# Optimization experiments

Measured on AMD Instinct MI355X. Metric: run time of the kernel, lower is better.

Reference implementation:

```python
import jax, jax.numpy as jnp
import numpy as np

K_ACT = 5          # k_active regimes
TAU = 0.5          # resample temperature
N = 8192           # n_particles (scaled to production size)
DZ, DM, KT, DE = 32, 64, 15, 16  # d_latent, d_mamba, k_regimes+10, d_regime_embed


def _lin(x, W, b):
    # torch nn.Linear convention: y = x @ W.T + b
    return x @ W.T + b


def setup_inputs() -> dict:
    key = jax.random.key(0)
    ks = iter(jax.random.split(key, 48))

    def rn(shape, s=1.0):
        return jax.random.normal(next(ks), shape, jnp.float32) * s

    inp = dict(
        remaining_high=jax.random.uniform(next(ks), (N,), jnp.float32) * 5.0 + 1.0,
        remaining_low=jax.random.uniform(next(ks), (N,), jnp.float32) * 5.0 + 1.0,
        z=rn((N, DZ)),
        regime_logits=rn((N, KT)),
        log_weights=rn((N,), 0.5),
        h_t=rn((DM,)),
        obs_remaining=jnp.float32(3.0),
        eps_high=rn((N,)),
        eps_low=rn((N,)),
        u_gumbel=jax.random.uniform(next(ks), (N, N), jnp.float32),
        embed=rn((KT, DE), 0.1),
        W_rt1=rn((32, DM + DE), 0.1), b_rt1=jnp.zeros(32, jnp.float32),
        W_rt2=rn((KT, 32), 0.1), b_rt2=jnp.zeros(KT, jnp.float32),
        W_d1=rn((64, DM + DE + DZ), 0.1), b_d1=jnp.zeros(64, jnp.float32),
        W_d2=rn((32, 64), 0.1), b_d2=jnp.zeros(32, jnp.float32),
        W_d3=rn((4, 32), 0.1), b_d3=jnp.zeros(4, jnp.float32),
        W_g=rn((DZ, DM + DE + DZ), 0.1), b_g=jnp.zeros(DZ, jnp.float32),
        W_c=rn((DZ, DM + DE + DZ), 0.1), b_c=jnp.zeros(DZ, jnp.float32),
        log_R=jnp.array([np.log(0.5), np.log(0.4), np.log(0.6)], jnp.float32),
        log_obs_scale=rn((KT,), 0.1),
        W_a1=rn((16, DM), 0.1), b_a1=jnp.zeros(16, jnp.float32),
        W_a2=rn((1, 16), 0.1), b_a2=jnp.zeros(1, jnp.float32),
    )
    return inp


def reference(remaining_high, remaining_low, z, regime_logits, log_weights, h_t,
              obs_remaining, eps_high, eps_low, u_gumbel, embed,
              W_rt1, b_rt1, W_rt2, b_rt2, W_d1, b_d1, W_d2, b_d2, W_d3, b_d3,
              W_g, b_g, W_c, b_c, log_R, log_obs_scale, W_a1, b_a1, W_a2, b_a2):
    silu = jax.nn.silu
    n = remaining_high.shape[0]
    h = jnp.broadcast_to(h_t, (n, h_t.shape[0]))  # (N, d_mamba)

    # ---- transition (predict step) ----
    rp = jax.nn.softmax(regime_logits, axis=-1)[:, :K_ACT]          # (N, K)
    remb = rp @ embed[:K_ACT]                                        # (N, d_embed)
    ri = jnp.concatenate([h, remb], axis=-1)                         # (N, 80)
    upd = _lin(silu(_lin(ri, W_rt1, b_rt1)), W_rt2, b_rt2)[:, :K_ACT]
    new_logits = regime_logits.at[:, :K_ACT].set(
        0.7 * regime_logits[:, :K_ACT] + 0.3 * upd)
    di = jnp.concatenate([h, remb, z], axis=-1)                      # (N, 112)
    dp = _lin(silu(_lin(silu(_lin(di, W_d1, b_d1)), W_d2, b_d2)), W_d3, b_d3)
    sig_h = jax.nn.softplus(dp[:, 2]) + 0.01
    sig_l = jax.nn.softplus(dp[:, 3]) + 0.01
    nh = jnp.clip(remaining_high + dp[:, 0] + sig_h * eps_high, 0.0)
    nl = jnp.clip(remaining_low + dp[:, 1] + sig_l * eps_low, 0.0)
    gate = jax.nn.sigmoid(_lin(di, W_g, b_g))
    nz = gate * z + (1.0 - gate) * jnp.tanh(_lin(di, W_c, b_c))

    # ---- observation: skew-normal log-likelihood (source_idx=0, 'high') ----
    R_src = jnp.clip(jnp.exp(log_R[0]), 0.15, 2.5)
    alpha = _lin(silu(_lin(h_t[None, :], W_a1, b_a1)), W_a2, b_a2)[0, 0]
    scales = jax.nn.softplus(log_obs_scale[:K_ACT])
    nrp = jax.nn.softmax(new_logits, axis=-1)[:, :K_ACT]
    R = jnp.clip(R_src * (nrp @ scales), 0.15, 4.0)                  # (N,)
    zz = (obs_remaining - nh) / R
    loglik = (jnp.log(2.0) - jnp.log(R) - 0.5 * jnp.log(2.0 * jnp.pi)
              - 0.5 * zz * zz + jax.scipy.stats.norm.logcdf(alpha * zz))

    # ---- weight update + normalization ----
    lw = log_weights + loglik
    lw = lw - jax.scipy.special.logsumexp(lw)

    # ---- soft resample (Gumbel-softmax relaxation) ----
    g = -jnp.log(-jnp.log(u_gumbel + 1e-10) + 1e-10)                 # (N, N)
    sa = jax.nn.softmax((lw[None, :] + g) / TAU, axis=-1)            # (N, N)
    state = jnp.concatenate([nh[:, None], nl[:, None], nz, new_logits], axis=-1)  # (N, 49)
    return sa @ state  # resampled [high | low | z | regime_logits]
```

## Files before the change

kernel.cpp:

```cpp
#include <hip/hip_runtime.h>
#include <math.h>

#define NP 8192

using f32x4  = __attribute__((ext_vector_type(4))) float;
using bf16x8 = __attribute__((ext_vector_type(8))) short;

__device__ __forceinline__ unsigned short f2bf(float x) {
  unsigned int u = __float_as_uint(x);
  u = (u + 0x7FFFu + ((u >> 16) & 1u)) >> 16;
  return (unsigned short)u;
}
__device__ __forceinline__ float fast_log2(float x) { float r; asm("v_log_f32 %0, %1" : "=v"(r) : "v"(x)); return r; }
__device__ __forceinline__ float fast_exp2(float x) { float r; asm("v_exp_f32 %0, %1" : "=v"(r) : "v"(x)); return r; }
__device__ __forceinline__ float siluf(float x) { return x / (1.0f + expf(-x)); }
__device__ __forceinline__ float softplusf(float x) { return (x > 20.0f) ? x : log1pf(expf(x)); }
__device__ __forceinline__ float dot4(const float4 a, const float4 b) {
  return a.x * b.x + a.y * b.y + a.z * b.z + a.w * b.w;
}


__global__ __launch_bounds__(128) void k_particle(
    const float* __restrict__ rh,   const float* __restrict__ rlo,
    const float* __restrict__ z,    const float* __restrict__ rlog,
    const float* __restrict__ logw, const float* __restrict__ h_t,
    const float* __restrict__ obs_p,
    const float* __restrict__ eps_h, const float* __restrict__ eps_l,
    const float* __restrict__ embed,
    const float* __restrict__ W_rt1, const float* __restrict__ b_rt1,
    const float* __restrict__ W_rt2, const float* __restrict__ b_rt2,
    const float* __restrict__ W_d1,  const float* __restrict__ b_d1,
    const float* __restrict__ W_d2,  const float* __restrict__ b_d2,
    const float* __restrict__ W_d3,  const float* __restrict__ b_d3,
    const float* __restrict__ W_g,   const float* __restrict__ b_g,
    const float* __restrict__ W_c,   const float* __restrict__ b_c,
    const float* __restrict__ log_R, const float* __restrict__ log_obs_scale,
    const float* __restrict__ W_a1,  const float* __restrict__ b_a1,
    const float* __restrict__ W_a2,  const float* __restrict__ b_a2,
    float* __restrict__ a_out, unsigned short* __restrict__ Bt) {
  __shared__ float d1c[64 * 48];
  __shared__ float gcs[32 * 48];
  __shared__ float ccs[32 * 48];
  __shared__ float rt1c[32 * 16];
  __shared__ float d2s[32 * 64];
  __shared__ float d3s[4 * 32];
  __shared__ float rt2s[5 * 32];
  __shared__ float embs[80];
  __shared__ float cD1[64], cRT1[32], cG[32], cC[32];
  __shared__ float bD2[32], bD3[4], bRT2[8];
  __shared__ float a1s[16], scal[8];
  __shared__ float x1ex[32 * 68];
  __shared__ float tx[32 * 36];
  __shared__ float stex[32 * 52];

  const int t = threadIdx.x;

#define STAGEM(DST, SRC, ROWS, SSTR, C0, NC)                          \
  for (int e = t; e < (ROWS) * (NC); e += 128) {                      \
    const int ro = e / (NC);                                          \
    const int co = e - ro * (NC);                                     \
    DST[e] = SRC[ro * (SSTR) + (C0) + co];                            \
  }
  STAGEM(d1c, W_d1, 64, 112, 64, 48)
  STAGEM(gcs, W_g, 32, 112, 64, 48)
  STAGEM(ccs, W_c, 32, 112, 64, 48)
  STAGEM(rt1c, W_rt1, 32, 80, 64, 16)
#undef STAGEM
  for (int e = t; e < 2048; e += 128) d2s[e] = W_d2[e];
  if (t < 128) d3s[t] = W_d3[t];
  for (int e = t; e < 160; e += 128) rt2s[e] = W_rt2[e];
  if (t < 80) embs[t] = embed[t];
  if (t < 32) bD2[t] = b_d2[t];
  if (t < 4)  bD3[t] = b_d3[t];
  if (t < 5)  bRT2[t] = b_rt2[t];

  for (int o = t; o < 160; o += 128) {
    const float* wr; float bb;
    if (o < 64)       { wr = W_d1 + o * 112;        bb = b_d1[o]; }
    else if (o < 96)  { wr = W_rt1 + (o - 64) * 80; bb = b_rt1[o - 64]; }
    else if (o < 128) { wr = W_g + (o - 96) * 112;  bb = b_g[o - 96]; }
    else              { wr = W_c + (o - 128) * 112; bb = b_c[o - 128]; }
    float acc = bb;
    #pragma unroll
    for (int m = 0; m < 64; m += 4)
      acc += dot4(*(const float4*)(wr + m), *(const float4*)(h_t + m));
    if (o < 64) cD1[o] = acc;
    else if (o < 96) cRT1[o - 64] = acc;
    else if (o < 128) cG[o - 96] = acc;
    else cC[o - 128] = acc;
  }
  if (t < 16) {
    float acc = b_a1[t];
    #pragma unroll
    for (int m = 0; m < 64; m += 4)
      acc += dot4(*(const float4*)(W_a1 + t * 64 + m), *(const float4*)(h_t + m));
    a1s[t] = siluf(acc);
  } else if (t == 16) {
    scal[1] = fminf(fmaxf(expf(log_R[0]), 0.15f), 2.5f);
  } else if (t >= 17 && t < 22) {
    scal[2 + t - 17] = softplusf(log_obs_scale[t - 17]);
  }
  __syncthreads();
  if (t == 0) {
    float acc = b_a2[0];
    #pragma unroll
    for (int k = 0; k < 16; ++k) acc += W_a2[k] * a1s[k];
    scal[0] = acc;
  }

  const int l = t & 63, lbase = l & ~3;
  const int q = t >> 2, s = t & 3;
  const int j = blockIdx.x * 32 + q;
  const float obs = obs_p[0];

  float rlj[15];
  #pragma unroll
  for (int k = 0; k < 15; ++k) rlj[k] = rlog[j * 15 + k];
  float m0 = rlj[0];
  #pragma unroll
  for (int k = 1; k < 15; ++k) m0 = fmaxf(m0, rlj[k]);
  float sum = 0.0f, e5[5];
  #pragma unroll
  for (int k = 0; k < 15; ++k) { float e = expf(rlj[k] - m0); if (k < 5) e5[k] = e; sum += e; }
  const float inv = 1.0f / sum;

  float remb[16];
  #pragma unroll
  for (int c = 0; c < 16; ++c) {
    float acc = e5[0] * embs[c];
    #pragma unroll
    for (int k = 1; k < 5; ++k) acc += e5[k] * embs[k * 16 + c];
    remb[c] = acc * inv;
  }

  float zj[32];
  #pragma unroll
  for (int c = 0; c < 32; c += 4) {
    const float4 v = *(const float4*)(z + j * 32 + c);
    zj[c] = v.x; zj[c + 1] = v.y; zj[c + 2] = v.z; zj[c + 3] = v.w;
  }

  #pragma unroll
  for (int r = 0; r < 8; ++r) {
    const int o = 4 * r + s;
    float acc = cRT1[o];
    #pragma unroll
    for (int c = 0; c < 16; ++c) acc += rt1c[o * 16 + c] * remb[c];
    tx[q * 36 + o] = siluf(acc);
  }
  __syncthreads();
  float t1[32];
  #pragma unroll
  for (int c = 0; c < 32; c += 4) {
    const float4 v = *(const float4*)(tx + q * 36 + c);
    t1[c] = v.x; t1[c + 1] = v.y; t1[c + 2] = v.z; t1[c + 3] = v.w;
  }
  float updS = bRT2[s], upd4 = bRT2[4];
  #pragma unroll
  for (int c = 0; c < 32; ++c) { updS += rt2s[s * 32 + c] * t1[c]; upd4 += rt2s[128 + c] * t1[c]; }
  float nlg[15];
  #pragma unroll
  for (int k = 0; k < 4; ++k) nlg[k] = 0.7f * rlj[k] + 0.3f * __shfl(updS, lbase + k);
  nlg[4] = 0.7f * rlj[4] + 0.3f * upd4;
  #pragma unroll
  for (int k = 5; k < 15; ++k) nlg[k] = rlj[k];

  #pragma unroll
  for (int r = 0; r < 16; ++r) {
    const int o = 4 * r + s;
    const float* wrow = d1c + o * 48;
    float acc = cD1[o];
    #pragma unroll
    for (int c = 0; c < 16; ++c) acc += wrow[c] * remb[c];
    #pragma unroll
    for (int c = 0; c < 32; ++c) acc += wrow[16 + c] * zj[c];
    x1ex[q * 68 + o] = siluf(acc);
  }
  __syncthreads();

  float acc8[8];
  #pragma unroll
  for (int r = 0; r < 8; ++r) acc8[r] = bD2[4 * r + s];
  #pragma unroll
  for (int half = 0; half < 2; ++half) {
    float xh[32];
    #pragma unroll
    for (int c = 0; c < 32; c += 4) {
      const float4 v = *(const float4*)(x1ex + q * 68 + half * 32 + c);
      xh[c] = v.x; xh[c + 1] = v.y; xh[c + 2] = v.z; xh[c + 3] = v.w;
    }
    #pragma unroll
    for (int r = 0; r < 8; ++r) {
      const int o = 4 * r + s;
      #pragma unroll
      for (int c = 0; c < 32; ++c) acc8[r] += d2s[o * 64 + half * 32 + c] * xh[c];
    }
  }
  #pragma unroll
  for (int r = 0; r < 8; ++r) tx[q * 36 + 4 * r + s] = siluf(acc8[r]);
  __syncthreads();
  float x2v[32];
  #pragma unroll
  for (int c = 0; c < 32; c += 4) {
    const float4 v = *(const float4*)(tx + q * 36 + c);
    x2v[c] = v.x; x2v[c + 1] = v.y; x2v[c + 2] = v.z; x2v[c + 3] = v.w;
  }
  float dps = bD3[s];
  #pragma unroll
  for (int c = 0; c < 32; ++c) dps += d3s[s * 32 + c] * x2v[c];
  const float dp0 = __shfl(dps, lbase), dp1 = __shfl(dps, lbase + 1);
  const float dp2 = __shfl(dps, lbase + 2), dp3 = __shfl(dps, lbase + 3);
  const float sig_h = softplusf(dp2) + 0.01f;
  const float sig_l = softplusf(dp3) + 0.01f;
  const float nh = fmaxf(rh[j] + dp0 + sig_h * eps_h[j], 0.0f);
  const float nl = fmaxf(rlo[j] + dp1 + sig_l * eps_l[j], 0.0f);

  #pragma unroll
  for (int r = 0; r < 8; ++r) {
    const int o = 4 * r + s;
    const float* gr = gcs + o * 48;
    const float* cr = ccs + o * 48;
    float ga = cG[o], caa = cC[o];
    #pragma unroll
    for (int c = 0; c < 16; ++c) { ga += gr[c] * remb[c]; caa += cr[c] * remb[c]; }
    #pragma unroll
    for (int c = 0; c < 32; ++c) { ga += gr[16 + c] * zj[c]; caa += cr[16 + c] * zj[c]; }
    const float gs = 1.0f / (1.0f + expf(-ga));
    stex[q * 52 + 2 + o] = gs * zj[o] + (1.0f - gs) * tanhf(caa);
  }

  if (s == 0) {
    stex[q * 52 + 0] = nh;
    stex[q * 52 + 1] = nl;
    #pragma unroll
    for (int k = 0; k < 15; ++k) stex[q * 52 + 34 + k] = nlg[k];
    float m1 = nlg[0];
    #pragma unroll
    for (int k = 1; k < 15; ++k) m1 = fmaxf(m1, nlg[k]);
    float sum1 = 0.0f, e5b[5];
    #pragma unroll
    for (int k = 0; k < 15; ++k) { float e = expf(nlg[k] - m1); if (k < 5) e5b[k] = e; sum1 += e; }
    float dot = 0.0f;
    #pragma unroll
    for (int k = 0; k < 5; ++k) dot += e5b[k] * scal[2 + k];
    dot /= sum1;
    const float R  = fminf(fmaxf(scal[1] * dot, 0.15f), 4.0f);
    const float zz = (obs - nh) / R;
    const float xx = scal[0] * zz;
    float lcdf;
    if (xx > -6.0f) {
      double p = 0.5 * erfc(-(double)xx * 0.7071067811865475244);
      lcdf = (float)log(p);
    } else {
      const float ix2 = 1.0f / (xx * xx);
      const float ser = 1.0f + ix2 * (-1.0f + ix2 * (3.0f + ix2 * (-15.0f + ix2 * 105.0f)));
      lcdf = -0.5f * xx * xx - logf(-xx) - 0.918938533f + logf(ser);
    }
    const float loglik = 0.693147181f - logf(R) - 0.918938533f - 0.5f * zz * zz + lcdf;
    a_out[j] = (logw[j] + loglik) * 2.8853900817779268f;
  }
  __syncthreads();

  if (t < 64) {
    const int c = t;
    const size_t base = (size_t)c * NP + (size_t)blockIdx.x * 32;
    if (c < 49) {
      #pragma unroll
      for (int e = 0; e < 4; ++e) {
        bf16x8 v8;
        #pragma unroll
        for (int r = 0; r < 8; ++r) v8[r] = (short)f2bf(stex[(8 * e + r) * 52 + c]);
        *(bf16x8*)(Bt + base + 8 * e) = v8;
      }
    } else if (c == 49) {
      bf16x8 v8;
      #pragma unroll
      for (int r = 0; r < 8; ++r) v8[r] = (short)0x3F80;
      #pragma unroll
      for (int e = 0; e < 4; ++e) *(bf16x8*)(Bt + base + 8 * e) = v8;
    } else {
      bf16x8 v8;
      #pragma unroll
      for (int r = 0; r < 8; ++r) v8[r] = 0;
      #pragma unroll
      for (int e = 0; e < 4; ++e) *(bf16x8*)(Bt + base + 8 * e) = v8;
    }
  }
}

__global__ __launch_bounds__(512) void k_resample(const float* __restrict__ u,
                                                  const float* __restrict__ a,
                                                  const unsigned short* __restrict__ Bt,
                                                  float* __restrict__ out) {
  __shared__ float cacc[8][64][16];
  __shared__ float zrow[16];
  const int t = threadIdx.x;
  const int w = t >> 6, l = t & 63;
  const int row = l & 15, kg = l >> 4;
  const int i0 = blockIdx.x << 4;
  const float* urow = u + (size_t)(i0 + row) * NP;
  const int jw = w << 10;

  f32x4 acc0 = {0.f, 0.f, 0.f, 0.f}, acc1 = acc0, acc2 = acc0, acc3 = acc0;

  #pragma unroll 2
  for (int kb = 0; kb < 32; ++kb) {
    const int jl = jw + (kb << 5) + (kg << 3);
    const float4 ua = *(const float4*)(urow + jl);
    const float4 ub = *(const float4*)(urow + jl + 4);
    const float4 aa = *(const float4*)(a + jl);
    const float4 ab = *(const float4*)(a + jl + 4);
    const float uu[8] = {ua.x, ua.y, ua.z, ua.w, ub.x, ub.y, ub.z, ub.w};
    const float av[8] = {aa.x, aa.y, aa.z, aa.w, ab.x, ab.y, ab.z, ab.w};
    bf16x8 af;
    #pragma unroll
    for (int e = 0; e < 8; ++e) {
      const float t1 = fast_log2(uu[e] + 1e-10f);
      const float t2 = fmaf(t1, -0.69314718056f, 1e-10f);
      const float t3 = fast_log2(t2);
      const float wv = fast_exp2(fmaf(t3, -2.0f, av[e]));
      af[e] = (short)f2bf(wv);
    }
    const bf16x8 b0 = *(const bf16x8*)(Bt + ((0  + row) * NP + jl));
    const bf16x8 b1 = *(const bf16x8*)(Bt + ((16 + row) * NP + jl));
    const bf16x8 b2 = *(const bf16x8*)(Bt + ((32 + row) * NP + jl));
    const bf16x8 b3 = *(const bf16x8*)(Bt + ((48 + row) * NP + jl));
    acc0 = __builtin_amdgcn_mfma_f32_16x16x32_bf16(af, b0, acc0, 0, 0, 0);
    acc1 = __builtin_amdgcn_mfma_f32_16x16x32_bf16(af, b1, acc1, 0, 0, 0);
    acc2 = __builtin_amdgcn_mfma_f32_16x16x32_bf16(af, b2, acc2, 0, 0, 0);
    acc3 = __builtin_amdgcn_mfma_f32_16x16x32_bf16(af, b3, acc3, 0, 0, 0);
  }

  #pragma unroll
  for (int r = 0; r < 4; ++r) {
    cacc[w][l][0 * 4 + r] = acc0[r];
    cacc[w][l][1 * 4 + r] = acc1[r];
    cacc[w][l][2 * 4 + r] = acc2[r];
    cacc[w][l][3 * 4 + r] = acc3[r];
  }
  __syncthreads();

  const int c = t & 63;
  float v[2];
  #pragma unroll
  for (int rr = 0; rr < 2; ++rr) {
    const int r    = ((t >> 6) << 1) + rr;
    const int lsrc = ((r >> 2) << 4) | (c & 15);
    const int reg  = ((c >> 4) << 2) + (r & 3);
    float sv = 0.0f;
    #pragma unroll
    for (int ww = 0; ww < 8; ++ww) sv += cacc[ww][lsrc][reg];
    v[rr] = sv;
    if (c == 49) zrow[r] = sv;
  }
  __syncthreads();
  if (c < 49) {
    #pragma unroll
    for (int rr = 0; rr < 2; ++rr) {
      const int r = ((t >> 6) << 1) + rr;
      out[(size_t)(i0 + r) * 49 + c] = v[rr] / zrow[r];
    }
  }
}

extern "C" void kernel_launch(void* const* d_in, const int* in_sizes, int n_in,
                              void* d_out, int out_size, void* d_ws, size_t ws_size,
                              hipStream_t stream) {
  const float* rh    = (const float*)d_in[0];
  const float* rlo   = (const float*)d_in[1];
  const float* z     = (const float*)d_in[2];
  const float* rlog  = (const float*)d_in[3];
  const float* logw  = (const float*)d_in[4];
  const float* h_t   = (const float*)d_in[5];
  const float* obs   = (const float*)d_in[6];
  const float* eps_h = (const float*)d_in[7];
  const float* eps_l = (const float*)d_in[8];
  const float* u     = (const float*)d_in[9];
  const float* embed = (const float*)d_in[10];
  const float* W_rt1 = (const float*)d_in[11];
  const float* b_rt1 = (const float*)d_in[12];
  const float* W_rt2 = (const float*)d_in[13];
  const float* b_rt2 = (const float*)d_in[14];
  const float* W_d1  = (const float*)d_in[15];
  const float* b_d1  = (const float*)d_in[16];
  const float* W_d2  = (const float*)d_in[17];
  const float* b_d2  = (const float*)d_in[18];
  const float* W_d3  = (const float*)d_in[19];
  const float* b_d3  = (const float*)d_in[20];
  const float* W_g   = (const float*)d_in[21];
  const float* b_g   = (const float*)d_in[22];
  const float* W_c   = (const float*)d_in[23];
  const float* b_c   = (const float*)d_in[24];
  const float* log_R = (const float*)d_in[25];
  const float* log_obs_scale = (const float*)d_in[26];
  const float* W_a1  = (const float*)d_in[27];
  const float* b_a1  = (const float*)d_in[28];
  const float* W_a2  = (const float*)d_in[29];
  const float* b_a2  = (const float*)d_in[30];

  float* ws_a = (float*)((char*)d_ws + 36864);
  unsigned short* ws_bt = (unsigned short*)((char*)d_ws + 73728);

  k_particle<<<256, 128, 0, stream>>>(rh, rlo, z, rlog, logw, h_t, obs, eps_h, eps_l,
                                      embed, W_rt1, b_rt1, W_rt2, b_rt2,
                                      W_d1, b_d1, W_d2, b_d2, W_d3, b_d3,
                                      W_g, b_g, W_c, b_c, log_R, log_obs_scale,
                                      W_a1, b_a1, W_a2, b_a2, ws_a, ws_bt);
  k_resample<<<512, 512, 0, stream>>>(u, ws_a, ws_bt, (float*)d_out);
}
```

Baseline: 526.1 us.

## Stage Gumbel weights through LDS and pre-swizzle B into MFMA fragment layout

The state matrix Bt is now written in a blocked layout so each wave reads its MFMA B fragments as contiguous 16-byte chunks per lane. The resample kernel now has all threads load u rows coalesced in 1024-column chunks, compute the Gumbel softmax weights, store them as bf16 in padded LDS, and then read A fragments from LDS. This replaces the earlier strided per-lane global loads of u and B with wide contiguous accesses. The cost is two block barriers per chunk and extra LDS traffic.

```diff
diff --git a/kernel.cpp b/kernel.cpp
--- a/kernel.cpp
+++ b/kernel.cpp
@@ -263,72 +263,88 @@
 
   if (t < 64) {
     const int c = t;
-    const size_t base = (size_t)c * NP + (size_t)blockIdx.x * 32;
+    const int b = c >> 4, rowc = c & 15;
     if (c < 49) {
       #pragma unroll
-      for (int e = 0; e < 4; ++e) {
+      for (int m = 0; m < 4; ++m) {
         bf16x8 v8;
         #pragma unroll
-        for (int r = 0; r < 8; ++r) v8[r] = (short)f2bf(stex[(8 * e + r) * 52 + c]);
-        *(bf16x8*)(Bt + base + 8 * e) = v8;
+        for (int r = 0; r < 8; ++r) v8[r] = (short)f2bf(stex[(8 * m + r) * 52 + c]);
+        *(bf16x8*)(Bt + (size_t)(((blockIdx.x * 4 + b) * 64) + m * 16 + rowc) * 8) = v8;
       }
     } else if (c == 49) {
       bf16x8 v8;
       #pragma unroll
       for (int r = 0; r < 8; ++r) v8[r] = (short)0x3F80;
       #pragma unroll
-      for (int e = 0; e < 4; ++e) *(bf16x8*)(Bt + base + 8 * e) = v8;
+      for (int m = 0; m < 4; ++m)
+        *(bf16x8*)(Bt + (size_t)(((blockIdx.x * 4 + b) * 64) + m * 16 + rowc) * 8) = v8;
     } else {
       bf16x8 v8;
       #pragma unroll
       for (int r = 0; r < 8; ++r) v8[r] = 0;
       #pragma unroll
-      for (int e = 0; e < 4; ++e) *(bf16x8*)(Bt + base + 8 * e) = v8;
+      for (int m = 0; m < 4; ++m)
+        *(bf16x8*)(Bt + (size_t)(((blockIdx.x * 4 + b) * 64) + m * 16 + rowc) * 8) = v8;
     }
   }
 }
 
+#define WSTR 1032
 __global__ __launch_bounds__(512) void k_resample(const float* __restrict__ u,
                                                   const float* __restrict__ a,
                                                   const unsigned short* __restrict__ Bt,
                                                   float* __restrict__ out) {
+  __shared__ unsigned short Wlds[16 * WSTR];
   __shared__ float cacc[8][64][16];
   __shared__ float zrow[16];
   const int t = threadIdx.x;
   const int w = t >> 6, l = t & 63;
-  const int row = l & 15, kg = l >> 4;
   const int i0 = blockIdx.x << 4;
-  const float* urow = u + (size_t)(i0 + row) * NP;
-  const int jw = w << 10;
 
   f32x4 acc0 = {0.f, 0.f, 0.f, 0.f}, acc1 = acc0, acc2 = acc0, acc3 = acc0;
 
-  #pragma unroll 2
-  for (int kb = 0; kb < 32; ++kb) {
-    const int jl = jw + (kb << 5) + (kg << 3);
-    const float4 ua = *(const float4*)(urow + jl);
-    const float4 ub = *(const float4*)(urow + jl + 4);
-    const float4 aa = *(const float4*)(a + jl);
-    const float4 ab = *(const float4*)(a + jl + 4);
-    const float uu[8] = {ua.x, ua.y, ua.z, ua.w, ub.x, ub.y, ub.z, ub.w};
-    const float av[8] = {aa.x, aa.y, aa.z, aa.w, ab.x, ab.y, ab.z, ab.w};
-    bf16x8 af;
-    #pragma unroll
-    for (int e = 0; e < 8; ++e) {
-      const float t1 = fast_log2(uu[e] + 1e-10f);
-      const float t2 = fmaf(t1, -0.69314718056f, 1e-10f);
-      const float t3 = fast_log2(t2);
-      const float wv = fast_exp2(fmaf(t3, -2.0f, av[e]));
-      af[e] = (short)f2bf(wv);
-    }
-    const bf16x8 b0 = *(const bf16x8*)(Bt + ((0  + row) * NP + jl));
-    const bf16x8 b1 = *(const bf16x8*)(Bt + ((16 + row) * NP + jl));
-    const bf16x8 b2 = *(const bf16x8*)(Bt + ((32 + row) * NP + jl));
-    const bf16x8 b3 = *(const bf16x8*)(Bt + ((48 + row) * NP + jl));
-    acc0 = __builtin_amdgcn_mfma_f32_16x16x32_bf16(af, b0, acc0, 0, 0, 0);
-    acc1 = __builtin_amdgcn_mfma_f32_16x16x32_bf16(af, b1, acc1, 0, 0, 0);
-    acc2 = __builtin_amdgcn_mfma_f32_16x16x32_bf16(af, b2, acc2, 0, 0, 0);
-    acc3 = __builtin_amdgcn_mfma_f32_16x16x32_bf16(af, b3, acc3, 0, 0, 0);
+  for (int chunk = 0; chunk < 8; ++chunk) {
+    const int c0 = chunk << 10;
+    #pragma unroll
+    for (int p = 0; p < 4; ++p) {
+      const int fidx = (p << 12) + (t << 3);
+      const int rr = fidx >> 10, col = fidx & 1023;
+      const float* up = u + (size_t)(i0 + rr) * NP + c0 + col;
+      const float4 ua = *(const float4*)(up);
+      const float4 ub = *(const float4*)(up + 4);
+      const float4 aa = *(const float4*)(a + c0 + col);
+      const float4 ab = *(const float4*)(a + c0 + col + 4);
+      const float uu[8] = {ua.x, ua.y, ua.z, ua.w, ub.x, ub.y, ub.z, ub.w};
+      const float av[8] = {aa.x, aa.y, aa.z, aa.w, ab.x, ab.y, ab.z, ab.w};
+      bf16x8 wv8;
+      #pragma unroll
+      for (int e = 0; e < 8; ++e) {
+        const float t1 = fast_log2(uu[e] + 1e-10f);
+        const float t2 = fmaf(t1, -0.69314718056f, 1e-10f);
+        const float t3 = fast_log2(t2);
+        const float wv = fast_exp2(fmaf(t3, -2.0f, av[e]));
+        wv8[e] = (short)f2bf(wv);
+      }
+      *(bf16x8*)(&Wlds[rr * WSTR + col]) = wv8;
+    }
+    __syncthreads();
+    #pragma unroll
+    for (int it = 0; it < 4; ++it) {
+      const int kb   = (w << 2) + it;
+      const int jblk = (c0 >> 5) + kb;
+      const bf16x8 af = *(const bf16x8*)(&Wlds[(l & 15) * WSTR + (kb << 5) + ((l >> 4) << 3)]);
+      const unsigned short* bp = Bt + (size_t)(jblk << 2) * 512;
+      const bf16x8 b0 = *(const bf16x8*)(bp + (0 * 64 + l) * 8);
+      const bf16x8 b1 = *(const bf16x8*)(bp + (1 * 64 + l) * 8);
+      const bf16x8 b2 = *(const bf16x8*)(bp + (2 * 64 + l) * 8);
+      const bf16x8 b3 = *(const bf16x8*)(bp + (3 * 64 + l) * 8);
+      acc0 = __builtin_amdgcn_mfma_f32_16x16x32_bf16(af, b0, acc0, 0, 0, 0);
+      acc1 = __builtin_amdgcn_mfma_f32_16x16x32_bf16(af, b1, acc1, 0, 0, 0);
+      acc2 = __builtin_amdgcn_mfma_f32_16x16x32_bf16(af, b2, acc2, 0, 0, 0);
+      acc3 = __builtin_amdgcn_mfma_f32_16x16x32_bf16(af, b3, acc3, 0, 0, 0);
+    }
+    __syncthreads();
   }
 
   #pragma unroll
```

Result: faster. 468.9 us (-10.9%).
